# Kernel tuning notes

Measured on AMD Instinct MI355X. Metric: run time of the kernel, lower is better.

## Reference

```python
import jax, jax.numpy as jnp
import numpy as np

NC = 64      # num_channels per whitening group
T = 5        # Newton-Schulz iterations
EPS = 1e-5


def setup_inputs() -> dict:
    key = jax.random.key(0)
    x = jax.random.normal(key, (64, 256, 56, 56), dtype=jnp.float32)
    weight = jnp.ones((1, 256, 1, 1), dtype=jnp.float32)
    bias = jnp.zeros((1, 256, 1, 1), dtype=jnp.float32)
    return {"x": x, "weight": weight, "bias": bias}


def _iternorm_whiten(X):
    B, C, H, W = X.shape
    g = C // NC
    # (g, nc, m) with m = B*H*W, matching X.transpose(0,1).view(g, nc, -1)
    xv = jnp.transpose(X, (1, 0, 2, 3)).reshape(g, NC, -1)
    m = xv.shape[-1]
    mean = xv.mean(-1, keepdims=True)          # (g, nc, 1)
    xc = xv - mean
    I = jnp.eye(NC, dtype=X.dtype)
    # Sigma = eps*I + xc @ xc^T / m   (baddbmm with beta=eps, alpha=1/m)
    Sigma = EPS * I + jnp.einsum('gdm,gem->gde', xc, xc) / m
    rTr = 1.0 / jnp.trace(Sigma, axis1=1, axis2=2)[:, None, None]  # (g,1,1)
    Sn = Sigma * rTr
    P = jnp.broadcast_to(I, (g, NC, NC))
    for _ in range(T):
        P3 = P @ P @ P
        P = 1.5 * P - 0.5 * (P3 @ Sn)
    wm = P * jnp.sqrt(rTr)                     # whitening matrix per group
    xn = wm @ xc                               # (g, nc, m)
    Xn = jnp.transpose(xn.reshape(C, B, H, W), (1, 0, 2, 3))
    return Xn


def reference(x, weight, bias):
    return _iternorm_whiten(x) * weight + bias
```

## Files before the change

kernel.cpp:

```cpp
#include <hip/hip_runtime.h>
#include <hip/hip_bf16.h>


#define B_    64
#define C_    256
#define HW_   3136
#define G_    4
#define NC_   64
#define M_    (B_*HW_)
#define EPS_  1e-5f
#define TIT_  5

#define NGB_  1024
#define PBLK_ 256

typedef __attribute__((ext_vector_type(8))) short  s16x8;
typedef __attribute__((ext_vector_type(4))) float  f32x4;

#define MFMA_(A,Bv,Cc) Cc = __builtin_amdgcn_mfma_f32_16x16x32_bf16(A, Bv, Cc, 0, 0, 0)

__device__ __forceinline__ unsigned short f2bf(float f){
  union{ float f; unsigned int u; } c; c.f = f;
  unsigned int u = c.u;
  u = u + 0x7FFFu + ((u >> 16) & 1u);
  return (unsigned short)(u >> 16);
}
__device__ __forceinline__ float bf2f(unsigned short h){
  union{ unsigned int u; float f; } c; c.u = ((unsigned int)h) << 16;
  return c.f;
}
__device__ __forceinline__ int swz(int off, int row){
  return off ^ ((row & 7) << 4) ^ (((row >> 3) & 3) << 5);
}
__device__ __forceinline__ s16x8 ld_frag(const unsigned short* base, int row, int kbyte){
  return *(const s16x8*)((const char*)base + swz(row*128 + kbyte, row));
}
__device__ __forceinline__ void st_h(unsigned short* base, int row, int col, unsigned short v){
  *(unsigned short*)((char*)base + swz(row*128 + col*2, row)) = v;
}
__device__ __forceinline__ unsigned short ld_h(const unsigned short* base, int row, int col){
  return *(const unsigned short*)((const char*)base + swz(row*128 + col*2, row));
}

template<bool ATOMIC>
__global__ __launch_bounds__(256) void k_gram(const float* __restrict__ x,
                                              float* __restrict__ S1,
                                              float* __restrict__ S2,
                                              float* __restrict__ partS2,
                                              float* __restrict__ partS1){
  __shared__ __align__(16) unsigned short tile[2][64*64];
  const int tid  = threadIdx.x;
  const int lane = tid & 63, wave = tid >> 6;
  const int bx   = blockIdx.x;
  const int g = bx >> 8, sub = bx & 255, b = sub >> 2, quad = sub & 3;
  const int ck0 = (quad*49) >> 2, ck1 = ((quad+1)*49) >> 2;
  const float* xg = x + ((size_t)b*C_ + (size_t)g*NC_) * HW_;
  const int chb = (tid >> 4) * 4;
  const int posoff = (tid & 15) * 4;
  const int wrow = (wave >> 1) * 32, wcol = (wave & 1) * 32;
  float s1a[4] = {0.f,0.f,0.f,0.f};
  f32x4 acc[2][2] = {};
  float v[4][4];

  auto load_c = [&](int ck){
    #pragma unroll
    for(int q = 0; q < 4; ++q){
      const float4 t = *(const float4*)(xg + (size_t)(chb+q)*HW_ + ck*64 + posoff);
      v[q][0]=t.x; v[q][1]=t.y; v[q][2]=t.z; v[q][3]=t.w;
    }
  };
  auto write_c = [&](unsigned short* tl){
    #pragma unroll
    for(int q = 0; q < 4; ++q){
      s1a[q] += v[q][0]+v[q][1]+v[q][2]+v[q][3];
      const int ch = chb + q;
      const unsigned long long pk =
            (unsigned long long)f2bf(v[q][0])
          | ((unsigned long long)f2bf(v[q][1]) << 16)
          | ((unsigned long long)f2bf(v[q][2]) << 32)
          | ((unsigned long long)f2bf(v[q][3]) << 48);
      *(unsigned long long*)((char*)tl + swz(ch*128 + posoff*2, ch)) = pk;
    }
  };
  auto comp = [&](const unsigned short* tl){
    #pragma unroll
    for(int ks = 0; ks < 2; ++ks){
      const int kbyte = ks*64 + (lane >> 4) * 16;
      s16x8 a0 = ld_frag(tl, wrow +      (lane & 15), kbyte);
      s16x8 a1 = ld_frag(tl, wrow + 16 + (lane & 15), kbyte);
      s16x8 b0 = ld_frag(tl, wcol +      (lane & 15), kbyte);
      s16x8 b1 = ld_frag(tl, wcol + 16 + (lane & 15), kbyte);
      MFMA_(a0, b0, acc[0][0]);
      MFMA_(a0, b1, acc[0][1]);
      MFMA_(a1, b0, acc[1][0]);
      MFMA_(a1, b1, acc[1][1]);
    }
  };

  load_c(ck0);
  write_c(tile[0]);
  __syncthreads();
  for(int ck = ck0; ck < ck1; ++ck){
    const int cur = (ck - ck0) & 1;
    const bool more = (ck + 1 < ck1);
    if(more) load_c(ck + 1);
    comp(tile[cur]);
    if(more) write_c(tile[cur ^ 1]);
    __syncthreads();
  }

  if(ATOMIC){
    float* S2g = S2 + g * (NC_*NC_);
    #pragma unroll
    for(int i = 0; i < 2; ++i)
    #pragma unroll
    for(int j = 0; j < 2; ++j)
    #pragma unroll
    for(int r = 0; r < 4; ++r){
      const int d = wrow + 16*i + (lane >> 4)*4 + r;
      const int e = wcol + 16*j + (lane & 15);
      atomicAdd(&S2g[d*NC_ + e], acc[i][j][r]);
    }
  }else{
    float* p2 = partS2 + (size_t)bx*4096 + tid*16;
    #pragma unroll
    for(int i = 0; i < 2; ++i)
    #pragma unroll
    for(int j = 0; j < 2; ++j)
      *(f32x4*)(p2 + (i*2+j)*4) = acc[i][j];
  }
  #pragma unroll
  for(int q = 0; q < 4; ++q){
    float s = s1a[q];
    #pragma unroll
    for(int m2 = 1; m2 < 16; m2 <<= 1) s += __shfl_xor(s, m2, 64);
    if((lane & 15) == 0){
      if(ATOMIC) atomicAdd(&S1[g*NC_ + chb + q], s);
      else       partS1[(size_t)bx*64 + chb + q] = s;
    }
  }
}

__global__ __launch_bounds__(256) void k_reduce(const float* __restrict__ partS2,
                                                const float* __restrict__ partS1,
                                                float* __restrict__ S1,
                                                float* __restrict__ S2){
  const int bid = blockIdx.x, tid = threadIdx.x;
  if(bid < 64){
    const int flat = bid*256 + tid;
    const int g = flat >> 12, t = flat & 4095;
    const float* p = partS2 + (size_t)(g*PBLK_)*4096 + t;
    float s = 0.f;
    for(int jb = 0; jb < PBLK_; ++jb) s += p[(size_t)jb*4096];
    const int tt = t >> 4, q = (t >> 2) & 3, r = t & 3;
    const int wave = tt >> 6, lane = tt & 63;
    const int d = (wave >> 1)*32 + ((q >> 1) << 4) + ((lane >> 4) << 2) + r;
    const int e = (wave &  1)*32 + ((q &  1) << 4) + (lane & 15);
    S2[g*4096 + d*64 + e] = s;
  }else{
    const int g = tid >> 6, ch = tid & 63;
    const float* p = partS1 + (size_t)(g*PBLK_)*64 + ch;
    float s = 0.f;
    for(int jb = 0; jb < PBLK_; ++jb) s += p[(size_t)jb*64];
    S1[tid] = s;
  }
}

__device__ __forceinline__ void mm_core(f32x4 acc[2][2],
    const unsigned short* Ah, const unsigned short* Al,
    const unsigned short* Bh, const unsigned short* Bl,
    int lane, int wrow, int wcol){
  #pragma unroll
  for(int ks = 0; ks < 2; ++ks){
    const int kbyte = ks*64 + (lane >> 4) * 16;
    s16x8 ah0 = ld_frag(Ah, wrow +      (lane & 15), kbyte);
    s16x8 ah1 = ld_frag(Ah, wrow + 16 + (lane & 15), kbyte);
    s16x8 al0 = ld_frag(Al, wrow +      (lane & 15), kbyte);
    s16x8 al1 = ld_frag(Al, wrow + 16 + (lane & 15), kbyte);
    s16x8 bh0 = ld_frag(Bh, wcol +      (lane & 15), kbyte);
    s16x8 bh1 = ld_frag(Bh, wcol + 16 + (lane & 15), kbyte);
    s16x8 bl0 = ld_frag(Bl, wcol +      (lane & 15), kbyte);
    s16x8 bl1 = ld_frag(Bl, wcol + 16 + (lane & 15), kbyte);
    MFMA_(ah0, bh0, acc[0][0]); MFMA_(ah0, bl0, acc[0][0]); MFMA_(al0, bh0, acc[0][0]);
    MFMA_(ah0, bh1, acc[0][1]); MFMA_(ah0, bl1, acc[0][1]); MFMA_(al0, bh1, acc[0][1]);
    MFMA_(ah1, bh0, acc[1][0]); MFMA_(ah1, bl0, acc[1][0]); MFMA_(al1, bh0, acc[1][0]);
    MFMA_(ah1, bh1, acc[1][1]); MFMA_(ah1, bl1, acc[1][1]); MFMA_(al1, bh1, acc[1][1]);
  }
}

__device__ __forceinline__ void mm64(unsigned short* dH, unsigned short* dL,
    const unsigned short* Ah, const unsigned short* Al,
    const unsigned short* Bh, const unsigned short* Bl,
    int lane, int wrow, int wcol){
  f32x4 acc[2][2] = {};
  mm_core(acc, Ah, Al, Bh, Bl, lane, wrow, wcol);
  #pragma unroll
  for(int i = 0; i < 2; ++i)
  #pragma unroll
  for(int j = 0; j < 2; ++j)
  #pragma unroll
  for(int r = 0; r < 4; ++r){
    const int d = wrow + 16*i + (lane >> 4)*4 + r;
    const int e = wcol + 16*j + (lane & 15);
    const float v = acc[i][j][r];
    const unsigned short h = f2bf(v);
    st_h(dH, d, e, h);
    st_h(dL, d, e, f2bf(v - bf2f(h)));
  }
}

__device__ __forceinline__ void ns_update(unsigned short* dH, unsigned short* dL,
    const unsigned short* Zh, const unsigned short* Zl,
    const unsigned short* Snh, const unsigned short* Snl,
    const unsigned short* pH, const unsigned short* pL,
    int lane, int wrow, int wcol){
  f32x4 acc[2][2] = {};
  mm_core(acc, Zh, Zl, Snh, Snl, lane, wrow, wcol);
  #pragma unroll
  for(int i = 0; i < 2; ++i)
  #pragma unroll
  for(int j = 0; j < 2; ++j)
  #pragma unroll
  for(int r = 0; r < 4; ++r){
    const int d = wrow + 16*i + (lane >> 4)*4 + r;
    const int e = wcol + 16*j + (lane & 15);
    const float pv = bf2f(ld_h(pH, d, e)) + bf2f(ld_h(pL, d, e));
    const float v = 1.5f*pv - 0.5f*acc[i][j][r];
    const unsigned short h = f2bf(v);
    st_h(dH, d, e, h);
    st_h(dL, d, e, f2bf(v - bf2f(h)));
  }
}

__global__ __launch_bounds__(256) void k_ns(const float* __restrict__ S1,
                                            const float* __restrict__ S2,
                                            const float* __restrict__ weight,
                                            const float* __restrict__ bias,
                                            float* __restrict__ wm,
                                            float* __restrict__ beta){
  __shared__ __align__(16) unsigned short smem[8*4096];
  unsigned short* Snh = smem;
  unsigned short* Snl = smem + 1*4096;
  unsigned short* Xh  = smem + 2*4096;
  unsigned short* Xl  = smem + 3*4096;
  unsigned short* Yh  = smem + 4*4096;
  unsigned short* Yl  = smem + 5*4096;
  unsigned short* Zh  = smem + 6*4096;
  unsigned short* Zl  = smem + 7*4096;
  const int g = blockIdx.x, tid = threadIdx.x;
  const int lane = tid & 63, wave = tid >> 6;
  const float* S1g = S1 + g*NC_;
  const float* S2g = S2 + g*NC_*NC_;
  const float invm = 1.0f / (float)M_;

  float term;
  {
    const float mui = S1g[lane] * invm;
    term = S2g[lane*NC_ + lane]*invm - mui*mui + EPS_;
    #pragma unroll
    for(int m2 = 1; m2 < 64; m2 <<= 1) term += __shfl_xor(term, m2, 64);
  }
  const float rTr  = 1.0f / term;
  const float srtr = sqrtf(rTr);

  {
    const int d  = tid >> 2;
    const int e0 = (tid & 3) * 16;
    const float mud = S1g[d] * invm;
    for(int k = 0; k < 16; ++k){
      const int e = e0 + k;
      const float mue = S1g[e] * invm;
      const float s = (S2g[d*NC_ + e]*invm - mud*mue + ((d==e)?EPS_:0.f)) * rTr;
      const unsigned short h = f2bf(s);
      st_h(Snh, d, e, h);
      st_h(Snl, d, e, f2bf(s - bf2f(h)));
      st_h(Xh,  d, e, (d==e)?(unsigned short)0x3F80:(unsigned short)0);
      st_h(Xl,  d, e, (unsigned short)0);
    }
  }
  __syncthreads();

  unsigned short *pH = Xh, *pL = Xl, *qH = Yh, *qL = Yl;
  const int wrow = (wave >> 1)*32, wcol = (wave & 1)*32;
  for(int it = 0; it < TIT_; ++it){
    mm64(qH, qL, pH, pL, pH, pL, lane, wrow, wcol);
    __syncthreads();
    mm64(Zh, Zl, qH, qL, pH, pL, lane, wrow, wcol);
    __syncthreads();
    ns_update(qH, qL, Zh, Zl, Snh, Snl, pH, pL, lane, wrow, wcol);
    __syncthreads();
    unsigned short* t;
    t = pH; pH = qH; qH = t;
    t = pL; pL = qL; qL = t;
  }

  float* wmg = wm + g*NC_*NC_;
  const int d  = tid >> 2;
  const int e0 = (tid & 3) * 16;
  float rs = 0.f;
  for(int k = 0; k < 16; ++k){
    const int e = e0 + k;
    const float wv = (bf2f(ld_h(pH, d, e)) + bf2f(ld_h(pL, d, e))) * srtr;
    wmg[d*NC_ + e] = wv;
    rs += wv * (S1g[e] * invm);
  }
  rs += __shfl_xor(rs, 1, 64);
  rs += __shfl_xor(rs, 2, 64);
  if((tid & 3) == 0)
    beta[g*NC_ + d] = bias[g*NC_ + d] - weight[g*NC_ + d] * rs;
}

__global__ __launch_bounds__(256, 8) void k_apply(const float* __restrict__ x,
                                                  const float* __restrict__ wm,
                                                  const float* __restrict__ beta,
                                                  const float* __restrict__ weight,
                                                  float* __restrict__ out){
  __shared__ __align__(16) unsigned short tileT[2][64*64];
  const int tid  = threadIdx.x;
  const int lane = tid & 63, wave = tid >> 6;
  const int bx   = blockIdx.x;
  const int g = bx >> 9, sub = bx & 511, b = sub >> 3, oct = sub & 7;
  const int ck0 = (oct*49) >> 3, ck1 = ((oct+1)*49) >> 3;
  const float* xg = x   + ((size_t)b*C_ + (size_t)g*NC_) * HW_;
  float*       og = out + ((size_t)b*C_ + (size_t)g*NC_) * HW_;
  const int chb = (tid >> 4) * 4;
  const int posoff = (tid & 15) * 4;

  const float* wmg = wm + g*NC_*NC_;
  const int arow = wave*16 + (lane & 15);
  s16x8 ah[2], al[2];
  #pragma unroll
  for(int ks = 0; ks < 2; ++ks){
    const int kc = ks*32 + (lane >> 4)*8;
    const float* p = wmg + arow*NC_ + kc;
    #pragma unroll
    for(int j = 0; j < 8; ++j){
      const float w = p[j];
      const unsigned short h = f2bf(w);
      ah[ks][j] = (short)h;
      al[ks][j] = (short)f2bf(w - bf2f(h));
    }
  }
  const int cl = wave*16 + (lane & 15);
  const float wt = weight[g*NC_ + cl];
  const float bt = beta  [g*NC_ + cl];

  float v[4][4];
  auto load_c = [&](int ck){
    #pragma unroll
    for(int q = 0; q < 4; ++q){
      const float4 t = *(const float4*)(xg + (size_t)(chb+q)*HW_ + ck*64 + posoff);
      v[q][0]=t.x; v[q][1]=t.y; v[q][2]=t.z; v[q][3]=t.w;
    }
  };
  auto write_c = [&](unsigned short* tl){
    #pragma unroll
    for(int r = 0; r < 4; ++r){
      const int p = posoff + r;
      const unsigned long long pk =
            (unsigned long long)f2bf(v[0][r])
          | ((unsigned long long)f2bf(v[1][r]) << 16)
          | ((unsigned long long)f2bf(v[2][r]) << 32)
          | ((unsigned long long)f2bf(v[3][r]) << 48);
      *(unsigned long long*)((char*)tl + p*128 + ((chb*2) ^ ((p & 7) << 4))) = pk;
    }
  };
  auto comp = [&](const unsigned short* tl, int p0){
    #pragma unroll
    for(int tn = 0; tn < 4; ++tn){
      f32x4 acc = {0.f,0.f,0.f,0.f};
      const int pos = tn*16 + (lane & 15);
      #pragma unroll
      for(int ks = 0; ks < 2; ++ks){
        const int cb = (ks*64 + (lane >> 4)*16) ^ ((pos & 7) << 4);
        const s16x8 afr = *(const s16x8*)((const char*)tl + pos*128 + cb);
        MFMA_(afr, ah[ks], acc);
        MFMA_(afr, al[ks], acc);
      }
      const int pr = p0 + tn*16 + ((lane >> 4) << 2);
      f32x4 o;
      o[0] = acc[0]*wt + bt;
      o[1] = acc[1]*wt + bt;
      o[2] = acc[2]*wt + bt;
      o[3] = acc[3]*wt + bt;
      __builtin_nontemporal_store(o, (f32x4*)(og + (size_t)cl*HW_ + pr));
    }
  };

  load_c(ck0);
  write_c(tileT[0]);
  __syncthreads();
  for(int ck = ck0; ck < ck1; ++ck){
    const int cur = (ck - ck0) & 1;
    const bool more = (ck + 1 < ck1);
    if(more) load_c(ck + 1);
    comp(tileT[cur], ck*64);
    if(more) write_c(tileT[cur ^ 1]);
    __syncthreads();
  }
}

extern "C" void kernel_launch(void* const* d_in, const int* in_sizes, int n_in,
                              void* d_out, int out_size, void* d_ws, size_t ws_size,
                              hipStream_t stream){
  (void)in_sizes; (void)n_in; (void)out_size;
  const float* x  = (const float*)d_in[0];
  const float* w  = (const float*)d_in[1];
  const float* bs = (const float*)d_in[2];
  float* out  = (float*)d_out;
  float* S1   = (float*)d_ws;
  float* S2   = S1 + 256;
  float* beta = S2 + G_*NC_*NC_;
  float* wm   = beta + 256;
  float* p2   = wm + G_*NC_*NC_;
  float* p1   = p2 + (size_t)NGB_*4096;
  const size_t need = ((size_t)(256 + G_*4096 + 256 + G_*4096)
                       + (size_t)NGB_*4096 + (size_t)NGB_*64) * sizeof(float);
  if(ws_size >= need){
    k_gram<false><<<NGB_, 256, 0, stream>>>(x, S1, S2, p2, p1);
    k_reduce<<<65, 256, 0, stream>>>(p2, p1, S1, S2);
  }else{
    hipError_t _e = hipMemsetAsync(d_ws, 0, (256 + G_*NC_*NC_)*sizeof(float), stream);
    (void)_e;
    k_gram<true><<<NGB_, 256, 0, stream>>>(x, S1, S2, p2, p1);
  }
  k_ns   <<<G_,   256, 0, stream>>>(S1, S2, w, bs, wm, beta);
  k_apply<<<2048, 256, 0, stream>>>(x, wm, beta, w, out);
}
```

Measured before the change: 168.6 us.

## Triple-buffer gram/apply tiles with two-ahead prefetch and parallelize partial reduction

The gram and apply kernels switch from double to triple LDS buffers. Global loads are now issued two chunks ahead, and the next tile is written before computing the current one, so load latency overlaps with more MFMA work. The reduce kernel splits each 256-long partial sum across 4 lanes with shuffle combining and launches 260 blocks instead of 65, which gives it more parallelism. The extra LDS raises per-block shared memory, and apply drops its occupancy hint of 8, so fewer blocks may be resident.

```diff
diff --git a/kernel.cpp b/kernel.cpp
--- a/kernel.cpp
+++ b/kernel.cpp
@@ -48,12 +48,13 @@
                                               float* __restrict__ S2,
                                               float* __restrict__ partS2,
                                               float* __restrict__ partS1){
-  __shared__ __align__(16) unsigned short tile[2][64*64];
+  __shared__ __align__(16) unsigned short tile[3][64*64];
   const int tid  = threadIdx.x;
   const int lane = tid & 63, wave = tid >> 6;
   const int bx   = blockIdx.x;
   const int g = bx >> 8, sub = bx & 255, b = sub >> 2, quad = sub & 3;
   const int ck0 = (quad*49) >> 2, ck1 = ((quad+1)*49) >> 2;
+  const int nck = ck1 - ck0;
   const float* xg = x + ((size_t)b*C_ + (size_t)g*NC_) * HW_;
   const int chb = (tid >> 4) * 4;
   const int posoff = (tid & 15) * 4;
@@ -99,13 +100,12 @@
 
   load_c(ck0);
   write_c(tile[0]);
+  if(nck > 1) load_c(ck0 + 1);
   __syncthreads();
-  for(int ck = ck0; ck < ck1; ++ck){
-    const int cur = (ck - ck0) & 1;
-    const bool more = (ck + 1 < ck1);
-    if(more) load_c(ck + 1);
-    comp(tile[cur]);
-    if(more) write_c(tile[cur ^ 1]);
+  for(int i = 0; i < nck; ++i){
+    if(i + 1 < nck) write_c(tile[(i+1)%3]);
+    if(i + 2 < nck) load_c(ck0 + i + 2);
+    comp(tile[i%3]);
     __syncthreads();
   }
 
@@ -146,23 +146,30 @@
                                                 float* __restrict__ S1,
                                                 float* __restrict__ S2){
   const int bid = blockIdx.x, tid = threadIdx.x;
-  if(bid < 64){
-    const int flat = bid*256 + tid;
+  const int sub = tid & 3;
+  if(bid < 256){
+    const int flat = (bid*256 + tid) >> 2;
     const int g = flat >> 12, t = flat & 4095;
-    const float* p = partS2 + (size_t)(g*PBLK_)*4096 + t;
+    const float* p = partS2 + ((size_t)(g*PBLK_ + sub*64))*4096 + t;
     float s = 0.f;
-    for(int jb = 0; jb < PBLK_; ++jb) s += p[(size_t)jb*4096];
-    const int tt = t >> 4, q = (t >> 2) & 3, r = t & 3;
-    const int wave = tt >> 6, lane = tt & 63;
-    const int d = (wave >> 1)*32 + ((q >> 1) << 4) + ((lane >> 4) << 2) + r;
-    const int e = (wave &  1)*32 + ((q &  1) << 4) + (lane & 15);
-    S2[g*4096 + d*64 + e] = s;
+    for(int jb = 0; jb < 64; ++jb) s += p[(size_t)jb*4096];
+    s += __shfl_xor(s, 1, 64);
+    s += __shfl_xor(s, 2, 64);
+    if(sub == 0){
+      const int tt = t >> 4, q = (t >> 2) & 3, r = t & 3;
+      const int wave = tt >> 6, lane = tt & 63;
+      const int d = (wave >> 1)*32 + ((q >> 1) << 4) + ((lane >> 4) << 2) + r;
+      const int e = (wave &  1)*32 + ((q &  1) << 4) + (lane & 15);
+      S2[g*4096 + d*64 + e] = s;
+    }
   }else{
-    const int g = tid >> 6, ch = tid & 63;
-    const float* p = partS1 + (size_t)(g*PBLK_)*64 + ch;
+    const int g = bid - 256, ch = tid >> 2;
+    const float* p = partS1 + ((size_t)(g*PBLK_ + sub*64))*64 + ch;
     float s = 0.f;
-    for(int jb = 0; jb < PBLK_; ++jb) s += p[(size_t)jb*64];
-    S1[tid] = s;
+    for(int jb = 0; jb < 64; ++jb) s += p[(size_t)jb*64];
+    s += __shfl_xor(s, 1, 64);
+    s += __shfl_xor(s, 2, 64);
+    if(sub == 0) S1[g*NC_ + ch] = s;
   }
 }
 
@@ -310,17 +317,18 @@
     beta[g*NC_ + d] = bias[g*NC_ + d] - weight[g*NC_ + d] * rs;
 }
 
-__global__ __launch_bounds__(256, 8) void k_apply(const float* __restrict__ x,
-                                                  const float* __restrict__ wm,
-                                                  const float* __restrict__ beta,
-                                                  const float* __restrict__ weight,
-                                                  float* __restrict__ out){
-  __shared__ __align__(16) unsigned short tileT[2][64*64];
+__global__ __launch_bounds__(256) void k_apply(const float* __restrict__ x,
+                                               const float* __restrict__ wm,
+                                               const float* __restrict__ beta,
+                                               const float* __restrict__ weight,
+                                               float* __restrict__ out){
+  __shared__ __align__(16) unsigned short tileT[3][64*64];
   const int tid  = threadIdx.x;
   const int lane = tid & 63, wave = tid >> 6;
   const int bx   = blockIdx.x;
   const int g = bx >> 9, sub = bx & 511, b = sub >> 3, oct = sub & 7;
   const int ck0 = (oct*49) >> 3, ck1 = ((oct+1)*49) >> 3;
+  const int nck = ck1 - ck0;
   const float* xg = x   + ((size_t)b*C_ + (size_t)g*NC_) * HW_;
   float*       og = out + ((size_t)b*C_ + (size_t)g*NC_) * HW_;
   const int chb = (tid >> 4) * 4;
@@ -389,13 +397,12 @@
 
   load_c(ck0);
   write_c(tileT[0]);
+  if(nck > 1) load_c(ck0 + 1);
   __syncthreads();
-  for(int ck = ck0; ck < ck1; ++ck){
-    const int cur = (ck - ck0) & 1;
-    const bool more = (ck + 1 < ck1);
-    if(more) load_c(ck + 1);
-    comp(tileT[cur], ck*64);
-    if(more) write_c(tileT[cur ^ 1]);
+  for(int i = 0; i < nck; ++i){
+    if(i + 1 < nck) write_c(tileT[(i+1)%3]);
+    if(i + 2 < nck) load_c(ck0 + i + 2);
+    comp(tileT[i%3], (ck0 + i)*64);
     __syncthreads();
   }
 }
@@ -418,7 +425,7 @@
                        + (size_t)NGB_*4096 + (size_t)NGB_*64) * sizeof(float);
   if(ws_size >= need){
     k_gram<false><<<NGB_, 256, 0, stream>>>(x, S1, S2, p2, p1);
-    k_reduce<<<65, 256, 0, stream>>>(p2, p1, S1, S2);
+    k_reduce<<<260, 256, 0, stream>>>(p2, p1, S1, S2);
   }else{
     hipError_t _e = hipMemsetAsync(d_ws, 0, (256 + G_*NC_*NC_)*sizeof(float), stream);
     (void)_e;
```

Result: faster. 150.4 us (-10.8%).
